# Performance work log

Measured on AMD Instinct MI355X. Metric: run time of the kernel, lower is better.

## Reference

```python
import jax, jax.numpy as jnp
import numpy as np

TEMPERATURE = 0.07
EPS = 1e-8  # torch F.cosine_similarity eps


def reference(z_i, z_j):
    N = z_i.shape[0]
    z = jnp.concatenate([z_i, z_j], axis=0)                      # [2N, D]
    norm = jnp.maximum(jnp.linalg.norm(z, axis=1, keepdims=True), EPS)
    zn = z / norm
    sim = (zn @ zn.T) / TEMPERATURE                              # [2N, 2N]
    n2 = 2 * N
    sim = jnp.where(jnp.eye(n2, dtype=bool), -jnp.inf, sim)      # mask self-sim
    lse = jax.scipy.special.logsumexp(sim, axis=1)               # [2N]
    idx = jnp.arange(N)
    # NT-Xent positives: row i (first half) pairs with col N+i; row N+i with col i
    pos_i = sim[idx, N + idx]
    pos_j = sim[N + idx, idx]
    loss_i = jnp.mean(lse[:N] - pos_i)
    loss_j = jnp.mean(lse[N:] - pos_j)
    return (loss_i + loss_j) / 2


def setup_inputs() -> dict:
    key = jax.random.key(0)
    k1, k2 = jax.random.split(key)
    N, D = 4096, 1024
    z_i = jax.random.normal(k1, (N, D), dtype=jnp.float32)
    z_j = jax.random.normal(k2, (N, D), dtype=jnp.float32)
    return {"z_i": z_i, "z_j": z_j}
```

## Files before the change

kernel.cpp:

```cpp
#include <hip/hip_runtime.h>
#include <hip/hip_bf16.h>
#include <stdint.h>
#include <math.h>


#define NROWS 8192
#define HALFN 4096
#define DIM   1024
#define INV_T 14.285714285714286f

typedef __bf16 bf16x8 __attribute__((ext_vector_type(8)));
typedef float  f32x4  __attribute__((ext_vector_type(4)));

__device__ __forceinline__ unsigned short f2bf(float x) {
  union { float f; uint32_t u; } c; c.f = x;
  uint32_t u = c.u;
  return (unsigned short)((u + 0x7FFFu + ((u >> 16) & 1u)) >> 16);
}

__device__ __forceinline__ void gload16(const void* g, void* lds) {
  __builtin_amdgcn_global_load_lds(
      (const __attribute__((address_space(1))) unsigned int*)g,
      (__attribute__((address_space(3))) unsigned int*)lds,
      16, 0, 0);
}

__global__ __launch_bounds__(256) void knorm(const float* __restrict__ zi,
                                             const float* __restrict__ zj,
                                             __bf16* __restrict__ znb,
                                             float* __restrict__ rnorm,
                                             float* __restrict__ rowsum,
                                             float* __restrict__ out) {
  int r = blockIdx.x;
  const float* z = (r < HALFN) ? (zi + (size_t)r * DIM)
                               : (zj + (size_t)(r - HALFN) * DIM);
  int t = threadIdx.x;
  float4 v = ((const float4*)z)[t];
  float ss = v.x*v.x + v.y*v.y + v.z*v.z + v.w*v.w;
  for (int m = 32; m; m >>= 1) ss += __shfl_xor(ss, m);
  __shared__ float wss[4];
  if ((t & 63) == 0) wss[t >> 6] = ss;
  __syncthreads();
  float nrm = sqrtf(wss[0] + wss[1] + wss[2] + wss[3]);
  nrm = fmaxf(nrm, 1e-8f);
  float rn = 1.0f / nrm;
  if (t == 0) {
    rnorm[r] = rn;
    rowsum[r] = 0.f;
    if (r == 0) out[0] = 0.f;
  }
  ushort4 o;
  o.x = f2bf(v.x * rn); o.y = f2bf(v.y * rn);
  o.z = f2bf(v.z * rn); o.w = f2bf(v.w * rn);
  ((ushort4*)znb)[(size_t)r * (DIM / 4) + t] = o;
}

__global__ __launch_bounds__(256, 3) void ksim(const __bf16* __restrict__ znb,
                                               float* __restrict__ rowsum) {
  __shared__ __align__(16) __bf16 As[128 * 32];
  __shared__ __align__(16) __bf16 Bs[128 * 32];

  unsigned bid = blockIdx.x;
  unsigned u = (bid & 7u) * 260u + (bid >> 3);
  int rbI = (int)(0.5f * (129.0f - sqrtf(16641.0f - 8.0f * (float)u)));
  while ((rbI + 1) * (129 - (rbI + 1)) / 2 <= (int)u) ++rbI;
  while (rbI * (129 - rbI) / 2 > (int)u) --rbI;
  int cbI = rbI + ((int)u - rbI * (129 - rbI) / 2);

  int t = threadIdx.x;
  int w = t >> 6, l = t & 63;
  int wr = w >> 1, wc = w & 1;
  int lr = l & 15, lg = l >> 4;

  const __bf16* Aor = znb + (size_t)rbI * 128 * DIM;
  const __bf16* Bor = znb + (size_t)cbI * 128 * DIM;

  int srow = l >> 2;
  int sck  = (l & 3) ^ ((l >> 3) & 3);
  int rsw  = (lr >> 1) & 3;

  f32x4 acc[4][4] = {};

  for (int kt = 0; kt < 32; ++kt) {
    int k0 = kt * 32;
#pragma unroll
    for (int i = 0; i < 2; ++i) {
      int row = i * 64 + w * 16 + srow;
      gload16(Aor + (size_t)row * DIM + k0 + sck * 8, (char*)As + i * 4096 + w * 1024);
      gload16(Bor + (size_t)row * DIM + k0 + sck * 8, (char*)Bs + i * 4096 + w * 1024);
    }
    __syncthreads();
    bf16x8 af[4], bg[4];
#pragma unroll
    for (int m = 0; m < 4; ++m) {
      int rowa = wr * 64 + m * 16 + lr;
      af[m] = *(const bf16x8*)((const char*)As + rowa * 64 + ((lg ^ rsw) * 16));
      int rowb = wc * 64 + m * 16 + lr;
      bg[m] = *(const bf16x8*)((const char*)Bs + rowb * 64 + ((lg ^ rsw) * 16));
    }
#pragma unroll
    for (int m = 0; m < 4; ++m)
#pragma unroll
      for (int n = 0; n < 4; ++n)
        acc[m][n] = __builtin_amdgcn_mfma_f32_16x16x32_bf16(af[m], bg[n], acc[m][n], 0, 0, 0);
    __syncthreads();
  }

  const float s2 = INV_T * 1.442695040888963f;
  int growb = rbI * 128 + wr * 64;
  int gcolb = cbI * 128 + wc * 64;
  float csn[4] = {0.f, 0.f, 0.f, 0.f};
#pragma unroll
  for (int m = 0; m < 4; ++m) {
    float s[4] = {0.f, 0.f, 0.f, 0.f};
#pragma unroll
    for (int n = 0; n < 4; ++n) {
      int gcol = gcolb + n * 16 + lr;
#pragma unroll
      for (int j = 0; j < 4; ++j) {
        int grow = growb + m * 16 + lg * 4 + j;
        float e = exp2f(fmaf(acc[m][n][j], s2, -s2));
        if (grow == gcol) e = 0.f;
        s[j] += e;
        csn[n] += e;
      }
    }
#pragma unroll
    for (int j = 0; j < 4; ++j) {
      float v = s[j];
      v += __shfl_xor(v, 1);
      v += __shfl_xor(v, 2);
      v += __shfl_xor(v, 4);
      v += __shfl_xor(v, 8);
      if (lr == 0)
        atomicAdd(rowsum + growb + m * 16 + lg * 4 + j, v);
    }
  }
  if (rbI != cbI) {
#pragma unroll
    for (int n = 0; n < 4; ++n) {
      float v = csn[n];
      v += __shfl_xor(v, 16);
      v += __shfl_xor(v, 32);
      if (lg == 0)
        atomicAdd(rowsum + gcolb + n * 16 + lr, v);
    }
  }
}

__global__ __launch_bounds__(256) void kfinal(const float* __restrict__ zi,
                                              const float* __restrict__ zj,
                                              const float* __restrict__ rnorm,
                                              const float* __restrict__ rowsum,
                                              float* __restrict__ out) {
  int t = threadIdx.x;
  int w = t >> 6, l = t & 63;
  float accum = 0.f;
#pragma unroll
  for (int sw = 0; sw < 4; ++sw) {
    int r = blockIdx.x * 4 + w + sw * 1024;
    const float* zr = zi + (size_t)r * DIM;
    const float* zp = zj + (size_t)r * DIM;
    float dot = 0.f;
#pragma unroll
    for (int j = 0; j < 4; ++j) {
      float4 a = ((const float4*)zr)[j * 64 + l];
      float4 b = ((const float4*)zp)[j * 64 + l];
      dot += a.x*b.x + a.y*b.y + a.z*b.z + a.w*b.w;
    }
    for (int m = 32; m; m >>= 1) dot += __shfl_xor(dot, m);
    if (l == 0) {
      float lse_r = logf(rowsum[r]) + INV_T;
      float lse_p = logf(rowsum[r + HALFN]) + INV_T;
      float pos = dot * rnorm[r] * rnorm[r + HALFN] * INV_T;
      accum += lse_r + lse_p - 2.0f * pos;
    }
  }
  __shared__ float part[4];
  if (l == 0) part[w] = accum;
  __syncthreads();
  if (t == 0)
    atomicAdd(out, (part[0] + part[1] + part[2] + part[3]) * (1.0f / (float)NROWS));
}

extern "C" void kernel_launch(void* const* d_in, const int* in_sizes, int n_in,
                              void* d_out, int out_size, void* d_ws, size_t ws_size,
                              hipStream_t stream) {
  const float* zi = (const float*)d_in[0];
  const float* zj = (const float*)d_in[1];
  float* out = (float*)d_out;
  char* ws = (char*)d_ws;
  __bf16* znb   = (__bf16*)ws;
  float*  rnorm = (float*)(ws + (size_t)NROWS * DIM * 2);
  float*  rowsum= (float*)(ws + (size_t)NROWS * DIM * 2 + NROWS * 4);

  knorm<<<NROWS, 256, 0, stream>>>(zi, zj, znb, rnorm, rowsum, out);
  ksim<<<2080, 256, 0, stream>>>(znb, rowsum);
  kfinal<<<256, 256, 0, stream>>>(zi, zj, rnorm, rowsum, out);
}
```

Before: 190.7 us.

## Use persistent atomic-counter tile scheduler and deepen K tile to 64

The similarity kernel becomes persistent: 768 blocks pull triangular tile indices from a global atomic counter, which knorm resets. This replaces the fixed grid of 2080 blocks and its XCD-interleaved mapping. The K step doubles from 32 to 64, with a matching 8-chunk XOR swizzle, which halves the number of barrier pairs per tile. The changes target wave-quantization tail imbalance and barrier overhead, at the cost of larger LDS use, an atomic per tile, and the loss of the XCD-aware L2 locality of the old block ordering.

```diff
diff --git a/kernel.cpp b/kernel.cpp
--- a/kernel.cpp
+++ b/kernel.cpp
@@ -7,6 +7,7 @@
 #define NROWS 8192
 #define HALFN 4096
 #define DIM   1024
+#define NTILES 2080
 #define INV_T 14.285714285714286f
 
 typedef __bf16 bf16x8 __attribute__((ext_vector_type(8)));
@@ -30,7 +31,8 @@
                                              __bf16* __restrict__ znb,
                                              float* __restrict__ rnorm,
                                              float* __restrict__ rowsum,
-                                             float* __restrict__ out) {
+                                             float* __restrict__ out,
+                                             unsigned* __restrict__ ctr) {
   int r = blockIdx.x;
   const float* z = (r < HALFN) ? (zi + (size_t)r * DIM)
                                : (zj + (size_t)(r - HALFN) * DIM);
@@ -47,7 +49,7 @@
   if (t == 0) {
     rnorm[r] = rn;
     rowsum[r] = 0.f;
-    if (r == 0) out[0] = 0.f;
+    if (r == 0) { out[0] = 0.f; ctr[0] = 0u; }
   }
   ushort4 o;
   o.x = f2bf(v.x * rn); o.y = f2bf(v.y * rn);
@@ -56,94 +58,109 @@
 }
 
 __global__ __launch_bounds__(256, 3) void ksim(const __bf16* __restrict__ znb,
-                                               float* __restrict__ rowsum) {
-  __shared__ __align__(16) __bf16 As[128 * 32];
-  __shared__ __align__(16) __bf16 Bs[128 * 32];
-
-  unsigned bid = blockIdx.x;
-  unsigned u = (bid & 7u) * 260u + (bid >> 3);
-  int rbI = (int)(0.5f * (129.0f - sqrtf(16641.0f - 8.0f * (float)u)));
-  while ((rbI + 1) * (129 - (rbI + 1)) / 2 <= (int)u) ++rbI;
-  while (rbI * (129 - rbI) / 2 > (int)u) --rbI;
-  int cbI = rbI + ((int)u - rbI * (129 - rbI) / 2);
+                                               float* __restrict__ rowsum,
+                                               unsigned* __restrict__ ctr) {
+  __shared__ __align__(16) __bf16 As[128 * 64];
+  __shared__ __align__(16) __bf16 Bs[128 * 64];
+  __shared__ unsigned s_u;
 
   int t = threadIdx.x;
   int w = t >> 6, l = t & 63;
   int wr = w >> 1, wc = w & 1;
   int lr = l & 15, lg = l >> 4;
 
-  const __bf16* Aor = znb + (size_t)rbI * 128 * DIM;
-  const __bf16* Bor = znb + (size_t)cbI * 128 * DIM;
-
-  int srow = l >> 2;
-  int sck  = (l & 3) ^ ((l >> 3) & 3);
-  int rsw  = (lr >> 1) & 3;
-
-  f32x4 acc[4][4] = {};
-
-  for (int kt = 0; kt < 32; ++kt) {
-    int k0 = kt * 32;
-#pragma unroll
-    for (int i = 0; i < 2; ++i) {
-      int row = i * 64 + w * 16 + srow;
-      gload16(Aor + (size_t)row * DIM + k0 + sck * 8, (char*)As + i * 4096 + w * 1024);
-      gload16(Bor + (size_t)row * DIM + k0 + sck * 8, (char*)Bs + i * 4096 + w * 1024);
-    }
+  int srow = l >> 3;
+  int sck  = (l & 7) ^ srow;
+  int rsw  = lr & 7;
+
+  const float s2 = INV_T * 1.442695040888963f;
+
+  for (;;) {
+    if (t == 0) s_u = atomicAdd(ctr, 1u);
     __syncthreads();
-    bf16x8 af[4], bg[4];
+    unsigned u = s_u;
+    if (u >= NTILES) return;
+
+    int rbI = (int)(0.5f * (129.0f - sqrtf(16641.0f - 8.0f * (float)u)));
+    while ((rbI + 1) * (129 - (rbI + 1)) / 2 <= (int)u) ++rbI;
+    while (rbI * (129 - rbI) / 2 > (int)u) --rbI;
+    int cbI = rbI + ((int)u - rbI * (129 - rbI) / 2);
+
+    const __bf16* Aor = znb + (size_t)rbI * 128 * DIM;
+    const __bf16* Bor = znb + (size_t)cbI * 128 * DIM;
+
+    f32x4 acc[4][4] = {};
+
+    for (int kt = 0; kt < 16; ++kt) {
+      int k0 = kt * 64;
+#pragma unroll
+      for (int j = 0; j < 4; ++j) {
+        int rowu = w * 32 + j * 8;
+        gload16(Aor + (size_t)(rowu + srow) * DIM + k0 + sck * 8,
+                (char*)As + rowu * 128);
+        gload16(Bor + (size_t)(rowu + srow) * DIM + k0 + sck * 8,
+                (char*)Bs + rowu * 128);
+      }
+      __syncthreads();
+#pragma unroll
+      for (int ks = 0; ks < 2; ++ks) {
+        bf16x8 af[4], bg[4];
+#pragma unroll
+        for (int m = 0; m < 4; ++m) {
+          int rowa = wr * 64 + m * 16 + lr;
+          af[m] = *(const bf16x8*)((const char*)As + rowa * 128 +
+                                   (((ks * 4 + lg) ^ rsw) * 16));
+          int rowb = wc * 64 + m * 16 + lr;
+          bg[m] = *(const bf16x8*)((const char*)Bs + rowb * 128 +
+                                   (((ks * 4 + lg) ^ rsw) * 16));
+        }
+#pragma unroll
+        for (int m = 0; m < 4; ++m)
+#pragma unroll
+          for (int n = 0; n < 4; ++n)
+            acc[m][n] = __builtin_amdgcn_mfma_f32_16x16x32_bf16(af[m], bg[n], acc[m][n], 0, 0, 0);
+      }
+      __syncthreads();
+    }
+
+    int growb = rbI * 128 + wr * 64;
+    int gcolb = cbI * 128 + wc * 64;
+    float csn[4] = {0.f, 0.f, 0.f, 0.f};
 #pragma unroll
     for (int m = 0; m < 4; ++m) {
-      int rowa = wr * 64 + m * 16 + lr;
-      af[m] = *(const bf16x8*)((const char*)As + rowa * 64 + ((lg ^ rsw) * 16));
-      int rowb = wc * 64 + m * 16 + lr;
-      bg[m] = *(const bf16x8*)((const char*)Bs + rowb * 64 + ((lg ^ rsw) * 16));
-    }
-#pragma unroll
-    for (int m = 0; m < 4; ++m)
-#pragma unroll
-      for (int n = 0; n < 4; ++n)
-        acc[m][n] = __builtin_amdgcn_mfma_f32_16x16x32_bf16(af[m], bg[n], acc[m][n], 0, 0, 0);
-    __syncthreads();
-  }
-
-  const float s2 = INV_T * 1.442695040888963f;
-  int growb = rbI * 128 + wr * 64;
-  int gcolb = cbI * 128 + wc * 64;
-  float csn[4] = {0.f, 0.f, 0.f, 0.f};
-#pragma unroll
-  for (int m = 0; m < 4; ++m) {
-    float s[4] = {0.f, 0.f, 0.f, 0.f};
-#pragma unroll
-    for (int n = 0; n < 4; ++n) {
-      int gcol = gcolb + n * 16 + lr;
+      float s[4] = {0.f, 0.f, 0.f, 0.f};
+#pragma unroll
+      for (int n = 0; n < 4; ++n) {
+        int gcol = gcolb + n * 16 + lr;
+#pragma unroll
+        for (int j = 0; j < 4; ++j) {
+          int grow = growb + m * 16 + lg * 4 + j;
+          float e = exp2f(fmaf(acc[m][n][j], s2, -s2));
+          if (grow == gcol) e = 0.f;
+          s[j] += e;
+          csn[n] += e;
+        }
+      }
 #pragma unroll
       for (int j = 0; j < 4; ++j) {
-        int grow = growb + m * 16 + lg * 4 + j;
-        float e = exp2f(fmaf(acc[m][n][j], s2, -s2));
-        if (grow == gcol) e = 0.f;
-        s[j] += e;
-        csn[n] += e;
-      }
-    }
-#pragma unroll
-    for (int j = 0; j < 4; ++j) {
-      float v = s[j];
-      v += __shfl_xor(v, 1);
-      v += __shfl_xor(v, 2);
-      v += __shfl_xor(v, 4);
-      v += __shfl_xor(v, 8);
-      if (lr == 0)
-        atomicAdd(rowsum + growb + m * 16 + lg * 4 + j, v);
-    }
-  }
-  if (rbI != cbI) {
-#pragma unroll
-    for (int n = 0; n < 4; ++n) {
-      float v = csn[n];
-      v += __shfl_xor(v, 16);
-      v += __shfl_xor(v, 32);
-      if (lg == 0)
-        atomicAdd(rowsum + gcolb + n * 16 + lr, v);
+        float v = s[j];
+        v += __shfl_xor(v, 1);
+        v += __shfl_xor(v, 2);
+        v += __shfl_xor(v, 4);
+        v += __shfl_xor(v, 8);
+        if (lr == 0)
+          atomicAdd(rowsum + growb + m * 16 + lg * 4 + j, v);
+      }
+    }
+    if (rbI != cbI) {
+#pragma unroll
+      for (int n = 0; n < 4; ++n) {
+        float v = csn[n];
+        v += __shfl_xor(v, 16);
+        v += __shfl_xor(v, 32);
+        if (lg == 0)
+          atomicAdd(rowsum + gcolb + n * 16 + lr, v);
+      }
     }
   }
 }
@@ -190,11 +207,12 @@
   const float* zj = (const float*)d_in[1];
   float* out = (float*)d_out;
   char* ws = (char*)d_ws;
-  __bf16* znb   = (__bf16*)ws;
-  float*  rnorm = (float*)(ws + (size_t)NROWS * DIM * 2);
-  float*  rowsum= (float*)(ws + (size_t)NROWS * DIM * 2 + NROWS * 4);
-
-  knorm<<<NROWS, 256, 0, stream>>>(zi, zj, znb, rnorm, rowsum, out);
-  ksim<<<2080, 256, 0, stream>>>(znb, rowsum);
+  __bf16* znb    = (__bf16*)ws;
+  float*  rnorm  = (float*)(ws + (size_t)NROWS * DIM * 2);
+  float*  rowsum = (float*)(ws + (size_t)NROWS * DIM * 2 + NROWS * 4);
+  unsigned* ctr  = (unsigned*)(ws + (size_t)NROWS * DIM * 2 + 2 * NROWS * 4);
+
+  knorm<<<NROWS, 256, 0, stream>>>(zi, zj, znb, rnorm, rowsum, out, ctr);
+  ksim<<<768, 256, 0, stream>>>(znb, rowsum, ctr);
   kfinal<<<256, 256, 0, stream>>>(zi, zj, rnorm, rowsum, out);
 }
```

After: 191.9 us. No clear change (+0.6%).
